# Optimization experiments

Measured on AMD Instinct MI355X. Metric: run time of the kernel, lower is better.

## Reference

```python
import jax, jax.numpy as jnp
import numpy as np

B, S = 4, 128
N_ITERS = 3  # original hardcodes range(3) regardless of max_iter


def _build_masks(edge_mask, chart_mask):
    S_ = edge_mask.shape[-1]
    ar = jnp.arange(S_)
    ne = ar[:, None] != ar[None, :]          # [a,b]: a != b
    le = ar[:, None] <= ar[None, :]
    ge = ar[:, None] >= ar[None, :]
    ls = jnp.minimum(ar[:, None], ar[None, :])  # min(a,b)
    rs = jnp.maximum(ar[:, None], ar[None, :])  # max(a,b)

    # edge_mask2o[b,h,m,s] = edge_mask[b,h,s] & edge_mask[b,h,m] & (m != s)
    em2o = edge_mask[:, :, None, :] & edge_mask[:, :, :, None]
    em2o = em2o & ne[None, None, :, :]
    # lrhs[h,m,s] = (min(m,s) >= h) | (max(m,s) <= h)
    lrhs = (ls[None, :, :] >= ar[:, None, None]) | (rs[None, :, :] <= ar[:, None, None])
    noncross = em2o & lrhs[None]
    # additionally require h != s for plain edge_mask2o
    em2o = em2o & ne[:, None, :][None]

    cm0 = chart_mask[:, 0]                                  # [B,S]
    pad = cm0[:, :, None] & cm0[:, None, :]                 # [B,S,S]
    chart_r = jnp.roll(chart_mask, 1, axis=1)               # cat((cm[:,-1:], cm[:,:-1]))
    # span_mask2o[b,i,j,s] = chart_r[b,i,j] & pad[b,j,s] & (max(i,j) != s)
    span2o = chart_r[:, :, :, None] & pad[:, None, :, :]
    span2o = span2o & (rs[:, :, None] != ar[None, None, :])[None]
    # inside[i,j,s] = (i <= s) & (j >= s)
    inside = le[:, None, :] & ge[None, :, :]
    outside = (~inside)[None] & span2o
    # off-diagonal pad mask: pad.triu(1) | pad.tril(-1) == pad & (i != j)
    outside = outside & (pad & ne[None])[:, :, :, None]
    return em2o, noncross, span2o, outside


def setup_inputs() -> dict:
    key = jax.random.key(0)
    ks = jax.random.split(key, 12)
    lens = jax.random.randint(ks[0], (B,), S // 2, S)
    valid = jnp.arange(S)[None, :] < lens[:, None]          # [B,S]
    edge_mask = valid[:, :, None] & valid[:, None, :]
    tri = jnp.triu(jnp.ones((S, S), dtype=bool), 1)
    chart_mask = edge_mask & tri[None]
    def rn(k, shape):
        return jax.random.normal(k, shape, dtype=jnp.float32)
    return {
        's_edge': rn(ks[1], (B, S, S)),
        's_const': rn(ks[2], (B, S, S)),
        's_sib': rn(ks[3], (B, S, S, S)),
        's_cop': rn(ks[4], (B, S, S, S)),
        's_grd': rn(ks[5], (B, S, S, S)),
        's_end_point': rn(ks[6], (B, S, S, S)),
        's_split': rn(ks[7], (B, S, S, S)),
        's_head_span_b': rn(ks[8], (B, S, S, S)),
        's_head_span_e': rn(ks[9], (B, S, S, S)),
        'edge_mask': edge_mask,
        'chart_mask': chart_mask,
    }


def reference(s_edge, s_const, s_sib, s_cop, s_grd, s_end_point, s_split,
              s_head_span_b, s_head_span_e, edge_mask, chart_mask):
    # symmetrize span scores: triu + triu(1).T on last two dims
    s_span = jnp.triu(s_const) + jnp.swapaxes(jnp.triu(s_const, 1), -1, -2)
    em2o, noncross, span2o, outside = _build_masks(edge_mask, chart_mask)

    s_sib = s_sib * em2o
    s_cop = s_cop * em2o
    s_grd = s_grd * em2o
    s_end_point = s_end_point * noncross
    s_split = s_split * span2o
    s_hb = s_head_span_b * outside
    s_he = jnp.transpose(s_head_span_e, (0, 2, 1, 3)) * outside

    # Note: the torch code aliases tmp_q_edge to s_edge and uses +=, so the
    # base scores accumulate across iterations; equivalently q <- q + update.
    q_edge, q_span = s_edge, s_span
    for _ in range(N_ITERS):
        pe = jax.nn.sigmoid(q_edge)
        ps = jax.nn.sigmoid(q_span)
        upd_e = (jnp.einsum('bhs,bhms->bhm', pe, s_sib)
                 + jnp.einsum('bsm,bhms->bhm', pe, s_cop)
                 + jnp.einsum('bms,bhms->bhm', ps, s_grd)
                 + jnp.einsum('bms,bhms->bhm', ps, s_end_point))
        upd_s = (jnp.einsum('bis,bijs->bis', ps, s_split)
                 + jnp.einsum('bsi,bijs->bij', pe, s_hb)
                 + jnp.einsum('bsj,bijs->bij', pe, s_he))
        q_edge = q_edge + upd_e
        q_span = q_span + upd_s
    return q_edge, q_span
```

## Files before the change

kernel.cpp:

```cpp
#include <hip/hip_runtime.h>
#include <stdint.h>

#define BB 4
#define SDIM 128
#define S2 (SDIM*SDIM)
#define S3 ((size_t)SDIM*S2)

__device__ __forceinline__ int probe_len(const void* em, int b, int lane) {
    const unsigned char* p8 = (const unsigned char*)em;
    const int* p32 = (const int*)em;
    const int t0 = lane, t1 = lane + 64;
    const size_t i0 = (size_t)b*S2 + (size_t)t0*SDIM + t0;
    const size_t i1 = (size_t)b*S2 + (size_t)t1*SDIM + t1;
    const unsigned char a0 = p8[i0], a1 = p8[i1];
    const bool ok = (a0 != 0) && (t1 != SDIM-1 || a1 == 0);
    const unsigned long long mok = __ballot(ok);
    const bool use8 = (mok == ~0ull);
    int v0, v1;
    if (use8) { v0 = (a0 != 0); v1 = (a1 != 0); }
    else      { v0 = (p32[i0] != 0); v1 = (p32[i1] != 0); }
    return __popcll(__ballot(v0)) + __popcll(__ballot(v1));
}

__global__ __launch_bounds__(256) void k_prep(
    const float* __restrict__ s_edge, const float* __restrict__ s_const,
    const float* __restrict__ s_split, const void* __restrict__ em,
    float* __restrict__ q_edge, float* __restrict__ q_span,
    float* __restrict__ splitsum) {
    const int b = blockIdx.x >> 7, i = blockIdx.x & 127;
    const int tid = threadIdx.x, lane = tid & 63;
    const int len = probe_len(em, b, lane);
    const size_t vb = (size_t)b*S2;
    if (tid < SDIM) {
        const size_t ro = vb + (size_t)i*SDIM + tid;
        q_edge[ro] = s_edge[ro];
        q_span[ro] = (i <= tid) ? s_const[ro] : s_const[vb + (size_t)tid*SDIM + i];
    }
    const int g = tid >> 5;
    const int kq = (tid & 31) * 4;
    float4 acc = make_float4(0.f, 0.f, 0.f, 0.f);
    if (i >= 1 && i < len && kq < len) {
        const float* base = s_split + (size_t)b*S3 + (size_t)i*S2;
        int j = i + g;
        for (; j + 24 < len; j += 32) {
            float4 v0 = *(const float4*)(base + (size_t)(j     )*SDIM + kq);
            float4 v1 = *(const float4*)(base + (size_t)(j +  8)*SDIM + kq);
            float4 v2 = *(const float4*)(base + (size_t)(j + 16)*SDIM + kq);
            float4 v3 = *(const float4*)(base + (size_t)(j + 24)*SDIM + kq);
            acc.x += ((j    != kq+0) ? v0.x : 0.f) + ((j+8  != kq+0) ? v1.x : 0.f)
                   + ((j+16 != kq+0) ? v2.x : 0.f) + ((j+24 != kq+0) ? v3.x : 0.f);
            acc.y += ((j    != kq+1) ? v0.y : 0.f) + ((j+8  != kq+1) ? v1.y : 0.f)
                   + ((j+16 != kq+1) ? v2.y : 0.f) + ((j+24 != kq+1) ? v3.y : 0.f);
            acc.z += ((j    != kq+2) ? v0.z : 0.f) + ((j+8  != kq+2) ? v1.z : 0.f)
                   + ((j+16 != kq+2) ? v2.z : 0.f) + ((j+24 != kq+2) ? v3.z : 0.f);
            acc.w += ((j    != kq+3) ? v0.w : 0.f) + ((j+8  != kq+3) ? v1.w : 0.f)
                   + ((j+16 != kq+3) ? v2.w : 0.f) + ((j+24 != kq+3) ? v3.w : 0.f);
        }
        for (; j < len; j += 8) {
            float4 v0 = *(const float4*)(base + (size_t)j*SDIM + kq);
            acc.x += (j != kq+0) ? v0.x : 0.f;
            acc.y += (j != kq+1) ? v0.y : 0.f;
            acc.z += (j != kq+2) ? v0.z : 0.f;
            acc.w += (j != kq+3) ? v0.w : 0.f;
        }
    }
    __shared__ float red[8][SDIM];
    *(float4*)&red[g][kq] = acc;
    __syncthreads();
    if (tid < SDIM) {
        float s = 0.f;
        #pragma unroll
        for (int gg = 0; gg < 8; ++gg) s += red[gg][tid];
        splitsum[vb + (size_t)i*SDIM + tid] = (tid >= 1 && tid < len) ? s : 0.f;
    }
}

__global__ void k_sig(const float* __restrict__ q_edge, const float* __restrict__ q_span,
                      float* __restrict__ pe, float* __restrict__ peT, float* __restrict__ ps) {
    int blk = blockIdx.x; int b = blk / SDIM; int r = blk % SDIM; int t = threadIdx.x;
    size_t o = (size_t)b*S2 + (size_t)r*SDIM + t;
    float v = 1.f / (1.f + expf(-q_edge[o]));
    pe[o] = v;
    peT[(size_t)b*S2 + (size_t)t*SDIM + r] = v;
    ps[o] = 1.f / (1.f + expf(-q_span[o]));
}

__global__ __launch_bounds__(256) void k_upd(
    const float* __restrict__ s_sib, const float* __restrict__ s_cop,
    const float* __restrict__ s_grd, const float* __restrict__ s_ep,
    const float* __restrict__ s_hb,  const float* __restrict__ s_he,
    const float* __restrict__ pe, const float* __restrict__ peT,
    const float* __restrict__ ps, const float* __restrict__ splitsum,
    const void* __restrict__ em,
    float* __restrict__ q_edge, float* __restrict__ q_span) {
    const int b = blockIdx.x >> 7, row = blockIdx.x & 127;
    const int tid = threadIdx.x, wave = tid >> 6, lane = tid & 63;
    const int half = lane >> 5, sq = (lane & 31) * 4;
    const int len = probe_len(em, b, lane);
    const int lm1 = len - 1;
    const int sqa = min(sq, lm1 & ~3);
    const size_t vb = (size_t)b*S2;

    if (blockIdx.y < 4) {
        const int h = row;
        if (h >= len) return;
        const int m0 = blockIdx.y * 32;
        if (m0 >= len) return;
        const size_t tb = (size_t)b*S3 + (size_t)h*S2;
        const float4 pe4 = *(const float4*)(pe + vb + (size_t)h*SDIM + sqa);
        int   mr[4];
        float4 sib[4], cop[4], grd[4], epv[4], pet[4], psv[4];
        #pragma unroll
        for (int it = 0; it < 4; ++it) {
            const int m = m0 + 8*it + 2*wave + half;
            mr[it] = m;
            const int mc = min(m, lm1);
            const size_t ro = tb + (size_t)mc*SDIM + sqa;
            sib[it] = *(const float4*)(s_sib + ro);
            cop[it] = *(const float4*)(s_cop + ro);
            grd[it] = *(const float4*)(s_grd + ro);
            epv[it] = *(const float4*)(s_ep  + ro);
            const size_t vo = vb + (size_t)mc*SDIM + sqa;
            pet[it] = *(const float4*)(peT + vo);
            psv[it] = *(const float4*)(ps  + vo);
        }
        #pragma unroll
        for (int it = 0; it < 4; ++it) {
            const int m = mr[it];
            const bool mv = (m < len);
            float r = 0.f;
            #define TERM(C, F) { const int s = sq + C;                               \
                const bool bs = mv && (s < len) && (m != s);                         \
                const float fem = (bs && (h != s)) ? 1.f : 0.f;                      \
                const float fnc = (bs && ((m >= h && s >= h) || (m <= h && s <= h))) \
                                  ? 1.f : 0.f;                                       \
                r += fem * (sib[it].F*pe4.F + cop[it].F*pet[it].F + grd[it].F*psv[it].F) \
                   + fnc * (epv[it].F*psv[it].F); }
            TERM(0, x) TERM(1, y) TERM(2, z) TERM(3, w)
            #undef TERM
            r += __shfl_xor(r, 16); r += __shfl_xor(r, 8); r += __shfl_xor(r, 4);
            r += __shfl_xor(r, 2);  r += __shfl_xor(r, 1);
            if ((lane & 31) == 0 && mv)
                q_edge[vb + (size_t)h*SDIM + m] += r;
        }
    } else {
        const int i = row;
        if (i < 1 || i >= len) return;
        const int j0 = (blockIdx.y - 4) * 32;
        if (j0 >= len) return;
        const float4 peTi4 = *(const float4*)(peT + vb + (size_t)i*SDIM + sqa);
        int jr[4];
        float4 hb[4], he[4], ptj[4];
        #pragma unroll
        for (int it = 0; it < 4; ++it) {
            const int j = j0 + 8*it + 2*wave + half;
            jr[it] = j;
            const int jc = min(j, lm1);
            hb[it]  = *(const float4*)(s_hb + (size_t)b*S3 + (size_t)i*S2 + (size_t)jc*SDIM + sqa);
            he[it]  = *(const float4*)(s_he + (size_t)b*S3 + (size_t)jc*S2 + (size_t)i*SDIM + sqa);
            ptj[it] = *(const float4*)(peT + vb + (size_t)jc*SDIM + sqa);
        }
        #pragma unroll
        for (int it = 0; it < 4; ++it) {
            const int j = jr[it];
            const bool act = (j > i) && (j < len);
            float r = 0.f;
            #define TERM(C, F) { const int s = sq + C;                               \
                const float f = (act && s >= 1 && s < len && (s < i || s > j))       \
                                ? 1.f : 0.f;                                         \
                r += f * (hb[it].F*peTi4.F + he[it].F*ptj[it].F); }
            TERM(0, x) TERM(1, y) TERM(2, z) TERM(3, w)
            #undef TERM
            r += __shfl_xor(r, 16); r += __shfl_xor(r, 8); r += __shfl_xor(r, 4);
            r += __shfl_xor(r, 2);  r += __shfl_xor(r, 1);
            if ((lane & 31) == 0 && j >= 1 && j < len) {
                const size_t qo = vb + (size_t)i*SDIM + j;
                q_span[qo] += r + ps[qo] * splitsum[qo];
            }
        }
    }
}

extern "C" void kernel_launch(void* const* d_in, const int* in_sizes, int n_in,
                              void* d_out, int out_size, void* d_ws, size_t ws_size,
                              hipStream_t stream) {
    const float* s_edge  = (const float*)d_in[0];
    const float* s_const = (const float*)d_in[1];
    const float* s_sib   = (const float*)d_in[2];
    const float* s_cop   = (const float*)d_in[3];
    const float* s_grd   = (const float*)d_in[4];
    const float* s_ep    = (const float*)d_in[5];
    const float* s_split = (const float*)d_in[6];
    const float* s_hb    = (const float*)d_in[7];
    const float* s_he    = (const float*)d_in[8];
    const void*  em      = d_in[9];
    (void)in_sizes; (void)n_in; (void)out_size; (void)ws_size;

    float* q_edge = (float*)d_out;
    float* q_span = q_edge + (size_t)BB * S2;

    char* ws = (char*)d_ws;
    float* splitsum = (float*)(ws);
    float* pe       = (float*)(ws + 1*(size_t)BB*S2*sizeof(float));
    float* peT      = (float*)(ws + 2*(size_t)BB*S2*sizeof(float));
    float* ps       = (float*)(ws + 3*(size_t)BB*S2*sizeof(float));

    const int NB = BB * SDIM;
    hipLaunchKernelGGL(k_prep, dim3(NB), dim3(256), 0, stream,
                       s_edge, s_const, s_split, em, q_edge, q_span, splitsum);
    for (int it = 0; it < 3; ++it) {
        hipLaunchKernelGGL(k_sig, dim3(NB), dim3(SDIM), 0, stream, q_edge, q_span, pe, peT, ps);
        hipLaunchKernelGGL(k_upd, dim3(dim3(NB, 8)), dim3(256), 0, stream,
                           s_sib, s_cop, s_grd, s_ep, s_hb, s_he,
                           pe, peT, ps, splitsum, em, q_edge, q_span);
    }
}
```

Before: 284.3 us.

## Fuse sigmoid into update kernel with ping-pong buffers and per-row software pipelining

Removes the separate sigmoid kernel by computing sigmoids of initial scores in the prep kernel and of updated scores at write time in the update kernel, using double-buffered pe/peT/ps arrays so reads and writes across iterations don't race. The update grid changes from 8 column-chunk blocks per row to 2 blocks per row (edge and span parts), each looping over all columns with a 4-deep register prefetch pipeline. This cuts kernel launches and one full pass over the probability arrays. In exchange there are fewer blocks and more serial work per block, which lowers parallelism for the bandwidth-bound 3D tensor reads.

```diff
diff --git a/kernel.cpp b/kernel.cpp
--- a/kernel.cpp
+++ b/kernel.cpp
@@ -22,19 +22,31 @@
     return __popcll(__ballot(v0)) + __popcll(__ballot(v1));
 }
 
+__device__ __forceinline__ float sigf(float x) { return 1.f / (1.f + expf(-x)); }
+
 __global__ __launch_bounds__(256) void k_prep(
     const float* __restrict__ s_edge, const float* __restrict__ s_const,
     const float* __restrict__ s_split, const void* __restrict__ em,
     float* __restrict__ q_edge, float* __restrict__ q_span,
-    float* __restrict__ splitsum) {
+    float* __restrict__ splitsum,
+    float* __restrict__ peA, float* __restrict__ peB,
+    float* __restrict__ peTA, float* __restrict__ peTB,
+    float* __restrict__ psA, float* __restrict__ psB) {
     const int b = blockIdx.x >> 7, i = blockIdx.x & 127;
     const int tid = threadIdx.x, lane = tid & 63;
     const int len = probe_len(em, b, lane);
     const size_t vb = (size_t)b*S2;
     if (tid < SDIM) {
         const size_t ro = vb + (size_t)i*SDIM + tid;
-        q_edge[ro] = s_edge[ro];
-        q_span[ro] = (i <= tid) ? s_const[ro] : s_const[vb + (size_t)tid*SDIM + i];
+        const float qe = s_edge[ro];
+        const float qs = (i <= tid) ? s_const[ro] : s_const[vb + (size_t)tid*SDIM + i];
+        q_edge[ro] = qe;
+        q_span[ro] = qs;
+        const float se = sigf(qe), ss = sigf(qs);
+        peA[ro] = se; peB[ro] = se;
+        psA[ro] = ss; psB[ro] = ss;
+        const size_t to = vb + (size_t)tid*SDIM + i;
+        peTA[to] = se; peTB[to] = se;
     }
     const int g = tid >> 5;
     const int kq = (tid & 31) * 4;
@@ -75,109 +87,133 @@
     }
 }
 
-__global__ void k_sig(const float* __restrict__ q_edge, const float* __restrict__ q_span,
-                      float* __restrict__ pe, float* __restrict__ peT, float* __restrict__ ps) {
-    int blk = blockIdx.x; int b = blk / SDIM; int r = blk % SDIM; int t = threadIdx.x;
-    size_t o = (size_t)b*S2 + (size_t)r*SDIM + t;
-    float v = 1.f / (1.f + expf(-q_edge[o]));
-    pe[o] = v;
-    peT[(size_t)b*S2 + (size_t)t*SDIM + r] = v;
-    ps[o] = 1.f / (1.f + expf(-q_span[o]));
-}
-
 __global__ __launch_bounds__(256) void k_upd(
     const float* __restrict__ s_sib, const float* __restrict__ s_cop,
     const float* __restrict__ s_grd, const float* __restrict__ s_ep,
     const float* __restrict__ s_hb,  const float* __restrict__ s_he,
-    const float* __restrict__ pe, const float* __restrict__ peT,
-    const float* __restrict__ ps, const float* __restrict__ splitsum,
+    const float* __restrict__ peA, const float* __restrict__ peTA,
+    const float* __restrict__ psA, const float* __restrict__ splitsum,
     const void* __restrict__ em,
-    float* __restrict__ q_edge, float* __restrict__ q_span) {
-    const int b = blockIdx.x >> 7, row = blockIdx.x & 127;
+    float* __restrict__ q_edge, float* __restrict__ q_span,
+    float* __restrict__ peB, float* __restrict__ peTB, float* __restrict__ psB) {
+    const int gid  = blockIdx.x;
+    const int part = gid & 1, b = (gid >> 1) & 3, row = gid >> 3;
     const int tid = threadIdx.x, wave = tid >> 6, lane = tid & 63;
     const int half = lane >> 5, sq = (lane & 31) * 4;
     const int len = probe_len(em, b, lane);
     const int lm1 = len - 1;
     const int sqa = min(sq, lm1 & ~3);
     const size_t vb = (size_t)b*S2;
-
-    if (blockIdx.y < 4) {
+    const int nst = (len + 7) >> 3;
+    const int nit = (nst + 3) & ~3;
+
+    if (part == 0) {
         const int h = row;
         if (h >= len) return;
-        const int m0 = blockIdx.y * 32;
-        if (m0 >= len) return;
         const size_t tb = (size_t)b*S3 + (size_t)h*S2;
-        const float4 pe4 = *(const float4*)(pe + vb + (size_t)h*SDIM + sqa);
-        int   mr[4];
-        float4 sib[4], cop[4], grd[4], epv[4], pet[4], psv[4];
-        #pragma unroll
-        for (int it = 0; it < 4; ++it) {
-            const int m = m0 + 8*it + 2*wave + half;
-            mr[it] = m;
-            const int mc = min(m, lm1);
-            const size_t ro = tb + (size_t)mc*SDIM + sqa;
-            sib[it] = *(const float4*)(s_sib + ro);
-            cop[it] = *(const float4*)(s_cop + ro);
-            grd[it] = *(const float4*)(s_grd + ro);
-            epv[it] = *(const float4*)(s_ep  + ro);
-            const size_t vo = vb + (size_t)mc*SDIM + sqa;
-            pet[it] = *(const float4*)(peT + vo);
-            psv[it] = *(const float4*)(ps  + vo);
-        }
-        #pragma unroll
-        for (int it = 0; it < 4; ++it) {
-            const int m = mr[it];
-            const bool mv = (m < len);
-            float r = 0.f;
-            #define TERM(C, F) { const int s = sq + C;                               \
-                const bool bs = mv && (s < len) && (m != s);                         \
-                const float fem = (bs && (h != s)) ? 1.f : 0.f;                      \
-                const float fnc = (bs && ((m >= h && s >= h) || (m <= h && s <= h))) \
-                                  ? 1.f : 0.f;                                       \
-                r += fem * (sib[it].F*pe4.F + cop[it].F*pet[it].F + grd[it].F*psv[it].F) \
-                   + fnc * (epv[it].F*psv[it].F); }
-            TERM(0, x) TERM(1, y) TERM(2, z) TERM(3, w)
-            #undef TERM
-            r += __shfl_xor(r, 16); r += __shfl_xor(r, 8); r += __shfl_xor(r, 4);
-            r += __shfl_xor(r, 2);  r += __shfl_xor(r, 1);
-            if ((lane & 31) == 0 && mv)
-                q_edge[vb + (size_t)h*SDIM + m] += r;
-        }
+        const size_t hrow = vb + (size_t)h*SDIM;
+        const float4 pe4 = *(const float4*)(peA + hrow + sqa);
+
+        float4 sib0,cop0,grd0,epv0,pet0,psv0; float qo0;
+        float4 sib1,cop1,grd1,epv1,pet1,psv1; float qo1;
+        float4 sib2,cop2,grd2,epv2,pet2,psv2; float qo2;
+        float4 sib3,cop3,grd3,epv3,pet3,psv3; float qo3;
+
+#define ELOAD(B, T) { \
+        const int tt = min((T), nst-1); \
+        const int mc_ = min(tt*8 + 2*wave + half, lm1); \
+        const size_t ro = tb + (size_t)mc_*SDIM + sqa; \
+        sib##B = *(const float4*)(s_sib + ro); \
+        cop##B = *(const float4*)(s_cop + ro); \
+        grd##B = *(const float4*)(s_grd + ro); \
+        epv##B = *(const float4*)(s_ep  + ro); \
+        const size_t vo = vb + (size_t)mc_*SDIM + sqa; \
+        pet##B = *(const float4*)(peTA + vo); \
+        psv##B = *(const float4*)(psA  + vo); \
+        qo##B  = q_edge[hrow + mc_]; }
+
+#define ETERM(B, C, F) { const int s = sq + C; \
+        const bool bs = mv && (s < len) && (m != s); \
+        const float fem = (bs && (h != s)) ? 1.f : 0.f; \
+        const float fnc = (bs && ((m >= h && s >= h) || (m <= h && s <= h))) \
+                          ? 1.f : 0.f; \
+        r += fem * (sib##B.F*pe4.F + cop##B.F*pet##B.F + grd##B.F*psv##B.F) \
+           + fnc * (epv##B.F*psv##B.F); }
+
+#define ECOMP(B, T) { \
+        const int m = (T)*8 + 2*wave + half; \
+        const bool mv = (m < len); \
+        float r = 0.f; \
+        ETERM(B,0,x) ETERM(B,1,y) ETERM(B,2,z) ETERM(B,3,w) \
+        r += __shfl_xor(r,16); r += __shfl_xor(r,8); r += __shfl_xor(r,4); \
+        r += __shfl_xor(r,2);  r += __shfl_xor(r,1); \
+        if ((lane & 31) == 0 && mv) { \
+            const float qn = qo##B + r; \
+            q_edge[hrow + m] = qn; \
+            const float sg = sigf(qn); \
+            peB[hrow + m] = sg; \
+            peTB[vb + (size_t)m*SDIM + h] = sg; } }
+
+        ELOAD(0,0) ELOAD(1,1) ELOAD(2,2) ELOAD(3,3)
+        for (int t = 0; t < nit; t += 4) {
+            const bool more = (t + 4 < nit);
+            ECOMP(0,t)   if (more) ELOAD(0,t+4)
+            ECOMP(1,t+1) if (more) ELOAD(1,t+5)
+            ECOMP(2,t+2) if (more) ELOAD(2,t+6)
+            ECOMP(3,t+3) if (more) ELOAD(3,t+7)
+        }
+#undef ELOAD
+#undef ETERM
+#undef ECOMP
     } else {
         const int i = row;
         if (i < 1 || i >= len) return;
-        const int j0 = (blockIdx.y - 4) * 32;
-        if (j0 >= len) return;
-        const float4 peTi4 = *(const float4*)(peT + vb + (size_t)i*SDIM + sqa);
-        int jr[4];
-        float4 hb[4], he[4], ptj[4];
-        #pragma unroll
-        for (int it = 0; it < 4; ++it) {
-            const int j = j0 + 8*it + 2*wave + half;
-            jr[it] = j;
-            const int jc = min(j, lm1);
-            hb[it]  = *(const float4*)(s_hb + (size_t)b*S3 + (size_t)i*S2 + (size_t)jc*SDIM + sqa);
-            he[it]  = *(const float4*)(s_he + (size_t)b*S3 + (size_t)jc*S2 + (size_t)i*SDIM + sqa);
-            ptj[it] = *(const float4*)(peT + vb + (size_t)jc*SDIM + sqa);
-        }
-        #pragma unroll
-        for (int it = 0; it < 4; ++it) {
-            const int j = jr[it];
-            const bool act = (j > i) && (j < len);
-            float r = 0.f;
-            #define TERM(C, F) { const int s = sq + C;                               \
-                const float f = (act && s >= 1 && s < len && (s < i || s > j))       \
-                                ? 1.f : 0.f;                                         \
-                r += f * (hb[it].F*peTi4.F + he[it].F*ptj[it].F); }
-            TERM(0, x) TERM(1, y) TERM(2, z) TERM(3, w)
-            #undef TERM
-            r += __shfl_xor(r, 16); r += __shfl_xor(r, 8); r += __shfl_xor(r, 4);
-            r += __shfl_xor(r, 2);  r += __shfl_xor(r, 1);
-            if ((lane & 31) == 0 && j >= 1 && j < len) {
-                const size_t qo = vb + (size_t)i*SDIM + j;
-                q_span[qo] += r + ps[qo] * splitsum[qo];
-            }
-        }
+        const size_t irow = vb + (size_t)i*SDIM;
+        const float4 peTi4 = *(const float4*)(peTA + irow + sqa);
+
+        float4 hb0,he0,ptj0; float qs0,pq0,ss0;
+        float4 hb1,he1,ptj1; float qs1,pq1,ss1;
+        float4 hb2,he2,ptj2; float qs2,pq2,ss2;
+        float4 hb3,he3,ptj3; float qs3,pq3,ss3;
+
+#define SLOAD(B, T) { \
+        const int tt = min((T), nst-1); \
+        const int jc_ = min(tt*8 + 2*wave + half, lm1); \
+        hb##B  = *(const float4*)(s_hb + (size_t)b*S3 + (size_t)i*S2 + (size_t)jc_*SDIM + sqa); \
+        he##B  = *(const float4*)(s_he + (size_t)b*S3 + (size_t)jc_*S2 + (size_t)i*SDIM + sqa); \
+        ptj##B = *(const float4*)(peTA + vb + (size_t)jc_*SDIM + sqa); \
+        qs##B  = q_span[irow + jc_]; \
+        pq##B  = psA[irow + jc_]; \
+        ss##B  = splitsum[irow + jc_]; }
+
+#define STERM(B, C, F) { const int s = sq + C; \
+        const float f = (act && s >= 1 && s < len && (s < i || s > j)) \
+                        ? 1.f : 0.f; \
+        r += f * (hb##B.F*peTi4.F + he##B.F*ptj##B.F); }
+
+#define SCOMP(B, T) { \
+        const int j = (T)*8 + 2*wave + half; \
+        const bool act = (j > i) && (j < len); \
+        float r = 0.f; \
+        STERM(B,0,x) STERM(B,1,y) STERM(B,2,z) STERM(B,3,w) \
+        r += __shfl_xor(r,16); r += __shfl_xor(r,8); r += __shfl_xor(r,4); \
+        r += __shfl_xor(r,2);  r += __shfl_xor(r,1); \
+        if ((lane & 31) == 0 && j >= 1 && j < len) { \
+            const float qn = qs##B + r + pq##B * ss##B; \
+            q_span[irow + j] = qn; \
+            psB[irow + j] = sigf(qn); } }
+
+        SLOAD(0,0) SLOAD(1,1) SLOAD(2,2) SLOAD(3,3)
+        for (int t = 0; t < nit; t += 4) {
+            const bool more = (t + 4 < nit);
+            SCOMP(0,t)   if (more) SLOAD(0,t+4)
+            SCOMP(1,t+1) if (more) SLOAD(1,t+5)
+            SCOMP(2,t+2) if (more) SLOAD(2,t+6)
+            SCOMP(3,t+3) if (more) SLOAD(3,t+7)
+        }
+#undef SLOAD
+#undef STERM
+#undef SCOMP
     }
 }
 
@@ -200,18 +236,30 @@
     float* q_span = q_edge + (size_t)BB * S2;
 
     char* ws = (char*)d_ws;
+    const size_t SZ = (size_t)BB * S2 * sizeof(float);
     float* splitsum = (float*)(ws);
-    float* pe       = (float*)(ws + 1*(size_t)BB*S2*sizeof(float));
-    float* peT      = (float*)(ws + 2*(size_t)BB*S2*sizeof(float));
-    float* ps       = (float*)(ws + 3*(size_t)BB*S2*sizeof(float));
+    float* peA  = (float*)(ws + 1*SZ);
+    float* peTA = (float*)(ws + 2*SZ);
+    float* psA  = (float*)(ws + 3*SZ);
+    float* peB  = (float*)(ws + 4*SZ);
+    float* peTB = (float*)(ws + 5*SZ);
+    float* psB  = (float*)(ws + 6*SZ);
 
     const int NB = BB * SDIM;
     hipLaunchKernelGGL(k_prep, dim3(NB), dim3(256), 0, stream,
-                       s_edge, s_const, s_split, em, q_edge, q_span, splitsum);
+                       s_edge, s_const, s_split, em, q_edge, q_span, splitsum,
+                       peA, peB, peTA, peTB, psA, psB);
     for (int it = 0; it < 3; ++it) {
-        hipLaunchKernelGGL(k_sig, dim3(NB), dim3(SDIM), 0, stream, q_edge, q_span, pe, peT, ps);
-        hipLaunchKernelGGL(k_upd, dim3(dim3(NB, 8)), dim3(256), 0, stream,
+        const int s = it & 1;
+        const float* peR  = s ? peB  : peA;
+        const float* peTR = s ? peTB : peTA;
+        const float* psR  = s ? psB  : psA;
+        float* peW  = s ? peA  : peB;
+        float* peTW = s ? peTA : peTB;
+        float* psW  = s ? psA  : psB;
+        hipLaunchKernelGGL(k_upd, dim3(2*NB), dim3(256), 0, stream,
                            s_sib, s_cop, s_grd, s_ep, s_hb, s_he,
-                           pe, peT, ps, splitsum, em, q_edge, q_span);
-    }
-}
+                           peR, peTR, psR, splitsum, em,
+                           q_edge, q_span, peW, peTW, psW);
+    }
+}
```

New measurement: 310.3 us. 1.09x slower.

## Fuse sigmoid into update kernel with ping-pong probability buffers

Applied to the files above, without the earlier changes.

Removes the standalone sigmoid kernel by computing sigmoids of the updated q_edge/q_span in the update kernel's writeback, using double-buffered pe/peT/ps arrays so readers see the previous iteration. The prep kernel now emits initial sigmoids and splits the split-score reduction over two y-blocks with fully unrolled clamped loads. Scheduling barriers group loads ahead of compute. This cuts per-iteration launches and intermediate traffic at the cost of more workspace and scattered transposed writes.

```diff
diff --git a/kernel.cpp b/kernel.cpp
--- a/kernel.cpp
+++ b/kernel.cpp
@@ -22,46 +22,57 @@
     return __popcll(__ballot(v0)) + __popcll(__ballot(v1));
 }
 
+__device__ __forceinline__ float sigf(float x) { return 1.f / (1.f + expf(-x)); }
+
 __global__ __launch_bounds__(256) void k_prep(
     const float* __restrict__ s_edge, const float* __restrict__ s_const,
     const float* __restrict__ s_split, const void* __restrict__ em,
     float* __restrict__ q_edge, float* __restrict__ q_span,
-    float* __restrict__ splitsum) {
+    float* __restrict__ split0, float* __restrict__ split1,
+    float* __restrict__ peA, float* __restrict__ peB,
+    float* __restrict__ peTA, float* __restrict__ peTB,
+    float* __restrict__ psA, float* __restrict__ psB) {
     const int b = blockIdx.x >> 7, i = blockIdx.x & 127;
+    const int y = blockIdx.y;
     const int tid = threadIdx.x, lane = tid & 63;
     const int len = probe_len(em, b, lane);
+    const int lm1 = len - 1;
     const size_t vb = (size_t)b*S2;
-    if (tid < SDIM) {
+    if (y == 0 && tid < SDIM) {
         const size_t ro = vb + (size_t)i*SDIM + tid;
-        q_edge[ro] = s_edge[ro];
-        q_span[ro] = (i <= tid) ? s_const[ro] : s_const[vb + (size_t)tid*SDIM + i];
+        const float qe = s_edge[ro];
+        const float qs = (i <= tid) ? s_const[ro] : s_const[vb + (size_t)tid*SDIM + i];
+        q_edge[ro] = qe;
+        q_span[ro] = qs;
+        const float se = sigf(qe), ss = sigf(qs);
+        peA[ro] = se; peB[ro] = se;
+        psA[ro] = ss; psB[ro] = ss;
+        const size_t to = vb + (size_t)tid*SDIM + i;
+        peTA[to] = se; peTB[to] = se;
     }
     const int g = tid >> 5;
     const int kq = (tid & 31) * 4;
     float4 acc = make_float4(0.f, 0.f, 0.f, 0.f);
     if (i >= 1 && i < len && kq < len) {
         const float* base = s_split + (size_t)b*S3 + (size_t)i*S2;
-        int j = i + g;
-        for (; j + 24 < len; j += 32) {
-            float4 v0 = *(const float4*)(base + (size_t)(j     )*SDIM + kq);
-            float4 v1 = *(const float4*)(base + (size_t)(j +  8)*SDIM + kq);
-            float4 v2 = *(const float4*)(base + (size_t)(j + 16)*SDIM + kq);
-            float4 v3 = *(const float4*)(base + (size_t)(j + 24)*SDIM + kq);
-            acc.x += ((j    != kq+0) ? v0.x : 0.f) + ((j+8  != kq+0) ? v1.x : 0.f)
-                   + ((j+16 != kq+0) ? v2.x : 0.f) + ((j+24 != kq+0) ? v3.x : 0.f);
-            acc.y += ((j    != kq+1) ? v0.y : 0.f) + ((j+8  != kq+1) ? v1.y : 0.f)
-                   + ((j+16 != kq+1) ? v2.y : 0.f) + ((j+24 != kq+1) ? v3.y : 0.f);
-            acc.z += ((j    != kq+2) ? v0.z : 0.f) + ((j+8  != kq+2) ? v1.z : 0.f)
-                   + ((j+16 != kq+2) ? v2.z : 0.f) + ((j+24 != kq+2) ? v3.z : 0.f);
-            acc.w += ((j    != kq+3) ? v0.w : 0.f) + ((j+8  != kq+3) ? v1.w : 0.f)
-                   + ((j+16 != kq+3) ? v2.w : 0.f) + ((j+24 != kq+3) ? v3.w : 0.f);
-        }
-        for (; j < len; j += 8) {
-            float4 v0 = *(const float4*)(base + (size_t)j*SDIM + kq);
-            acc.x += (j != kq+0) ? v0.x : 0.f;
-            acc.y += (j != kq+1) ? v0.y : 0.f;
-            acc.z += (j != kq+2) ? v0.z : 0.f;
-            acc.w += (j != kq+3) ? v0.w : 0.f;
+        const int j0 = i + g + 8*y;
+        float4 v[8]; int jv[8];
+        #pragma unroll
+        for (int t = 0; t < 8; ++t) {
+            const int j = j0 + 16*t;
+            jv[t] = j;
+            const int jc = min(j, lm1);
+            v[t] = *(const float4*)(base + (size_t)jc*SDIM + kq);
+        }
+        __builtin_amdgcn_sched_barrier(0);
+        #pragma unroll
+        for (int t = 0; t < 8; ++t) {
+            const int j = jv[t];
+            const bool jb = (j < len);
+            acc.x += (jb && j != kq+0) ? v[t].x : 0.f;
+            acc.y += (jb && j != kq+1) ? v[t].y : 0.f;
+            acc.z += (jb && j != kq+2) ? v[t].z : 0.f;
+            acc.w += (jb && j != kq+3) ? v[t].w : 0.f;
         }
     }
     __shared__ float red[8][SDIM];
@@ -71,28 +82,21 @@
         float s = 0.f;
         #pragma unroll
         for (int gg = 0; gg < 8; ++gg) s += red[gg][tid];
-        splitsum[vb + (size_t)i*SDIM + tid] = (tid >= 1 && tid < len) ? s : 0.f;
-    }
-}
-
-__global__ void k_sig(const float* __restrict__ q_edge, const float* __restrict__ q_span,
-                      float* __restrict__ pe, float* __restrict__ peT, float* __restrict__ ps) {
-    int blk = blockIdx.x; int b = blk / SDIM; int r = blk % SDIM; int t = threadIdx.x;
-    size_t o = (size_t)b*S2 + (size_t)r*SDIM + t;
-    float v = 1.f / (1.f + expf(-q_edge[o]));
-    pe[o] = v;
-    peT[(size_t)b*S2 + (size_t)t*SDIM + r] = v;
-    ps[o] = 1.f / (1.f + expf(-q_span[o]));
+        float* out = y ? split1 : split0;
+        out[vb + (size_t)i*SDIM + tid] = (tid >= 1 && tid < len) ? s : 0.f;
+    }
 }
 
 __global__ __launch_bounds__(256) void k_upd(
     const float* __restrict__ s_sib, const float* __restrict__ s_cop,
     const float* __restrict__ s_grd, const float* __restrict__ s_ep,
     const float* __restrict__ s_hb,  const float* __restrict__ s_he,
-    const float* __restrict__ pe, const float* __restrict__ peT,
-    const float* __restrict__ ps, const float* __restrict__ splitsum,
+    const float* __restrict__ peA, const float* __restrict__ peTA,
+    const float* __restrict__ psA,
+    const float* __restrict__ split0, const float* __restrict__ split1,
     const void* __restrict__ em,
-    float* __restrict__ q_edge, float* __restrict__ q_span) {
+    float* __restrict__ q_edge, float* __restrict__ q_span,
+    float* __restrict__ peB, float* __restrict__ peTB, float* __restrict__ psB) {
     const int b = blockIdx.x >> 7, row = blockIdx.x & 127;
     const int tid = threadIdx.x, wave = tid >> 6, lane = tid & 63;
     const int half = lane >> 5, sq = (lane & 31) * 4;
@@ -107,9 +111,11 @@
         const int m0 = blockIdx.y * 32;
         if (m0 >= len) return;
         const size_t tb = (size_t)b*S3 + (size_t)h*S2;
-        const float4 pe4 = *(const float4*)(pe + vb + (size_t)h*SDIM + sqa);
+        const size_t hrow = vb + (size_t)h*SDIM;
+        const float4 pe4 = *(const float4*)(peA + hrow + sqa);
         int   mr[4];
         float4 sib[4], cop[4], grd[4], epv[4], pet[4], psv[4];
+        float qo[4];
         #pragma unroll
         for (int it = 0; it < 4; ++it) {
             const int m = m0 + 8*it + 2*wave + half;
@@ -121,9 +127,11 @@
             grd[it] = *(const float4*)(s_grd + ro);
             epv[it] = *(const float4*)(s_ep  + ro);
             const size_t vo = vb + (size_t)mc*SDIM + sqa;
-            pet[it] = *(const float4*)(peT + vo);
-            psv[it] = *(const float4*)(ps  + vo);
-        }
+            pet[it] = *(const float4*)(peTA + vo);
+            psv[it] = *(const float4*)(psA  + vo);
+            qo[it]  = q_edge[hrow + mc];
+        }
+        __builtin_amdgcn_sched_barrier(0);
         #pragma unroll
         for (int it = 0; it < 4; ++it) {
             const int m = mr[it];
@@ -140,17 +148,24 @@
             #undef TERM
             r += __shfl_xor(r, 16); r += __shfl_xor(r, 8); r += __shfl_xor(r, 4);
             r += __shfl_xor(r, 2);  r += __shfl_xor(r, 1);
-            if ((lane & 31) == 0 && mv)
-                q_edge[vb + (size_t)h*SDIM + m] += r;
+            if ((lane & 31) == 0 && mv) {
+                const float qn = qo[it] + r;
+                q_edge[hrow + m] = qn;
+                const float sg = sigf(qn);
+                peB[hrow + m] = sg;
+                peTB[vb + (size_t)m*SDIM + h] = sg;
+            }
         }
     } else {
         const int i = row;
         if (i < 1 || i >= len) return;
         const int j0 = (blockIdx.y - 4) * 32;
         if (j0 >= len) return;
-        const float4 peTi4 = *(const float4*)(peT + vb + (size_t)i*SDIM + sqa);
+        const size_t irow = vb + (size_t)i*SDIM;
+        const float4 peTi4 = *(const float4*)(peTA + irow + sqa);
         int jr[4];
         float4 hb[4], he[4], ptj[4];
+        float qs[4], pq[4], s0[4], s1[4];
         #pragma unroll
         for (int it = 0; it < 4; ++it) {
             const int j = j0 + 8*it + 2*wave + half;
@@ -158,8 +173,13 @@
             const int jc = min(j, lm1);
             hb[it]  = *(const float4*)(s_hb + (size_t)b*S3 + (size_t)i*S2 + (size_t)jc*SDIM + sqa);
             he[it]  = *(const float4*)(s_he + (size_t)b*S3 + (size_t)jc*S2 + (size_t)i*SDIM + sqa);
-            ptj[it] = *(const float4*)(peT + vb + (size_t)jc*SDIM + sqa);
-        }
+            ptj[it] = *(const float4*)(peTA + vb + (size_t)jc*SDIM + sqa);
+            qs[it]  = q_span[irow + jc];
+            pq[it]  = psA[irow + jc];
+            s0[it]  = split0[irow + jc];
+            s1[it]  = split1[irow + jc];
+        }
+        __builtin_amdgcn_sched_barrier(0);
         #pragma unroll
         for (int it = 0; it < 4; ++it) {
             const int j = jr[it];
@@ -174,8 +194,9 @@
             r += __shfl_xor(r, 16); r += __shfl_xor(r, 8); r += __shfl_xor(r, 4);
             r += __shfl_xor(r, 2);  r += __shfl_xor(r, 1);
             if ((lane & 31) == 0 && j >= 1 && j < len) {
-                const size_t qo = vb + (size_t)i*SDIM + j;
-                q_span[qo] += r + ps[qo] * splitsum[qo];
+                const float qn = qs[it] + r + pq[it] * (s0[it] + s1[it]);
+                q_span[irow + j] = qn;
+                psB[irow + j] = sigf(qn);
             }
         }
     }
@@ -200,18 +221,31 @@
     float* q_span = q_edge + (size_t)BB * S2;
 
     char* ws = (char*)d_ws;
-    float* splitsum = (float*)(ws);
-    float* pe       = (float*)(ws + 1*(size_t)BB*S2*sizeof(float));
-    float* peT      = (float*)(ws + 2*(size_t)BB*S2*sizeof(float));
-    float* ps       = (float*)(ws + 3*(size_t)BB*S2*sizeof(float));
+    const size_t SZ = (size_t)BB * S2 * sizeof(float);
+    float* split0 = (float*)(ws);
+    float* split1 = (float*)(ws + 1*SZ);
+    float* peA    = (float*)(ws + 2*SZ);
+    float* peTA   = (float*)(ws + 3*SZ);
+    float* psA    = (float*)(ws + 4*SZ);
+    float* peB    = (float*)(ws + 5*SZ);
+    float* peTB   = (float*)(ws + 6*SZ);
+    float* psB    = (float*)(ws + 7*SZ);
 
     const int NB = BB * SDIM;
-    hipLaunchKernelGGL(k_prep, dim3(NB), dim3(256), 0, stream,
-                       s_edge, s_const, s_split, em, q_edge, q_span, splitsum);
+    hipLaunchKernelGGL(k_prep, dim3(NB, 2), dim3(256), 0, stream,
+                       s_edge, s_const, s_split, em, q_edge, q_span,
+                       split0, split1, peA, peB, peTA, peTB, psA, psB);
     for (int it = 0; it < 3; ++it) {
-        hipLaunchKernelGGL(k_sig, dim3(NB), dim3(SDIM), 0, stream, q_edge, q_span, pe, peT, ps);
+        const int s = it & 1;
+        const float* peR  = s ? peB  : peA;
+        const float* peTR = s ? peTB : peTA;
+        const float* psR  = s ? psB  : psA;
+        float* peW  = s ? peA  : peB;
+        float* peTW = s ? peTA : peTB;
+        float* psW  = s ? psA  : psB;
         hipLaunchKernelGGL(k_upd, dim3(dim3(NB, 8)), dim3(256), 0, stream,
                            s_sib, s_cop, s_grd, s_ep, s_hb, s_he,
-                           pe, peT, ps, splitsum, em, q_edge, q_span);
-    }
-}
+                           peR, peTR, psR, split0, split1, em,
+                           q_edge, q_span, peW, peTW, psW);
+    }
+}
```

Measured after the change: 278.6 us. 1.02x faster.
